# Performance work log

Hardware: AMD Instinct MI355X
Metric: run time of the kernel (lower is better)

Reference implementation:

```python
import jax, jax.numpy as jnp
import numpy as np

D_MODEL = 768
N_HEADS_CFG = 12
D_STATE = 32
D_CONV = 4
EXPAND = 2
HEADDIM = D_MODEL // N_HEADS_CFG          # 64
D_INNER = EXPAND * D_MODEL                # 1536
NHEADS = D_INNER // HEADDIM               # 24 (Mamba2 internal heads)
CONV_DIM = D_INNER + 2 * D_STATE          # 1600
D_IN_PROJ = 2 * D_INNER + 2 * D_STATE + NHEADS  # 3160
EPS = 1e-5
B_SZ, SEQ = 2, 512


def rmsnorm(x, w):
    return x * jax.lax.rsqrt(jnp.mean(x * x, axis=-1, keepdims=True) + EPS) * w


def mamba2(u, Wi, cw, cb, dtb, Alog, Dp, nw, Wo):
    """Mamba2 mixer: in_proj -> causal depthwise conv(silu) -> selective scan -> gated RMSNorm -> out_proj."""
    b, l, _ = u.shape
    zxbcdt = u @ Wi.T                                   # [b,l,d_in_proj]
    z, xBC, dt = jnp.split(zxbcdt, [D_INNER, D_INNER + CONV_DIM], axis=-1)
    # causal depthwise conv over time
    xBC = jnp.transpose(xBC, (0, 2, 1))                 # [b,c,l]
    xBC = jax.lax.conv_general_dilated(
        xBC, cw[:, None, :], window_strides=(1,),
        padding=[(D_CONV - 1, 0)], feature_group_count=CONV_DIM)
    xBC = jax.nn.silu(jnp.transpose(xBC + cb[None, :, None], (0, 2, 1)))
    x, Bm, Cm = jnp.split(xBC, [D_INNER, D_INNER + D_STATE], axis=-1)
    x = x.reshape(b, l, NHEADS, HEADDIM)                # [b,l,h,p]
    dt = jax.nn.softplus(dt + dtb)                      # [b,l,h]
    A = -jnp.exp(Alog)                                  # [h]
    a = jnp.exp(dt * A)                                 # decay [b,l,h]
    # dt * x outer B  -> [b,l,h,p,n]
    dBx = (dt[..., None, None] * x[..., None]) * Bm[:, :, None, None, :]

    def combine(e1, e2):
        a1, h1 = e1
        a2, h2 = e2
        return (a1 * a2, a2[..., None, None] * h1 + h2)

    _, h = jax.lax.associative_scan(combine, (a, dBx), axis=1)  # h: [b,l,h,p,n]
    y = jnp.einsum('blhpn,bln->blhp', h, Cm) + Dp[None, None, :, None] * x
    y = y.reshape(b, l, D_INNER)
    y = rmsnorm(y * jax.nn.silu(z), nw)                 # gated RMSNorm
    return y @ Wo.T                                     # [b,l,d_model]


def _mamba_params(key, scale=0.02):
    ks = jax.random.split(key, 6)
    return dict(
        in_w=jax.random.normal(ks[0], (D_IN_PROJ, D_MODEL), jnp.float32) * scale,
        conv_w=jax.random.normal(ks[1], (CONV_DIM, D_CONV), jnp.float32) * scale,
        conv_b=jnp.zeros((CONV_DIM,), jnp.float32),
        dt_bias=jax.random.uniform(ks[2], (NHEADS,), jnp.float32, -4.0, -1.0),
        A_log=jnp.log(jax.random.uniform(ks[3], (NHEADS,), jnp.float32, 1.0, 16.0)),
        D=jnp.ones((NHEADS,), jnp.float32),
        norm_w=jnp.ones((D_INNER,), jnp.float32),
        out_w=jax.random.normal(ks[4], (D_MODEL, D_INNER), jnp.float32) * scale,
    )


def setup_inputs() -> dict:
    key = jax.random.key(0)
    kx, kf, kb, ko = jax.random.split(key, 4)
    f = _mamba_params(kf)
    bw = _mamba_params(kb)
    return {
        'x': jax.random.normal(kx, (B_SZ, SEQ, D_MODEL), jnp.float32),
        'norm_w': jnp.ones((D_MODEL,), jnp.float32),
        'fwd_in_w': f['in_w'], 'fwd_conv_w': f['conv_w'], 'fwd_conv_b': f['conv_b'],
        'fwd_dt_bias': f['dt_bias'], 'fwd_A_log': f['A_log'], 'fwd_D': f['D'],
        'fwd_norm_w': f['norm_w'], 'fwd_out_w': f['out_w'],
        'bwd_in_w': bw['in_w'], 'bwd_conv_w': bw['conv_w'], 'bwd_conv_b': bw['conv_b'],
        'bwd_dt_bias': bw['dt_bias'], 'bwd_A_log': bw['A_log'], 'bwd_D': bw['D'],
        'bwd_norm_w': bw['norm_w'], 'bwd_out_w': bw['out_w'],
        'out_proj_w': jax.random.normal(ko, (D_MODEL, 2 * D_MODEL), jnp.float32) * 0.02,
    }


def reference(x, norm_w,
              fwd_in_w, fwd_conv_w, fwd_conv_b, fwd_dt_bias, fwd_A_log, fwd_D, fwd_norm_w, fwd_out_w,
              bwd_in_w, bwd_conv_w, bwd_conv_b, bwd_dt_bias, bwd_A_log, bwd_D, bwd_norm_w, bwd_out_w,
              out_proj_w):
    h = rmsnorm(x, norm_w)
    f_out = mamba2(h, fwd_in_w, fwd_conv_w, fwd_conv_b, fwd_dt_bias, fwd_A_log, fwd_D, fwd_norm_w, fwd_out_w)
    b_out = mamba2(h[:, ::-1], bwd_in_w, bwd_conv_w, bwd_conv_b, bwd_dt_bias, bwd_A_log, bwd_D, bwd_norm_w, bwd_out_w)[:, ::-1]
    return x + jnp.concatenate([f_out, b_out], axis=-1) @ out_proj_w.T
```

## Files before the change

### kernel.cpp

```cpp
#include <hip/hip_runtime.h>
#include <hip/hip_bf16.h>

#define DMODEL 768
#define DINNER 1536
#define DSTATE 32
#define NHEADS 24
#define HEADDIM 64
#define CONVDIM 1600
#define DINPROJ 3160
#define NPAD 3200
#define SEQ 512
#define MROWS 1024
#define CL 64
#define NCH 8

typedef __attribute__((ext_vector_type(8))) short bf16x8;
typedef __attribute__((ext_vector_type(4))) float f32x4;

__device__ __forceinline__ ushort f2bs(float v) {
  __hip_bfloat16 b = __float2bfloat16(v);
  return __builtin_bit_cast(unsigned short, b);
}

__device__ __forceinline__ void gld16(const void* g, const void* l) {
  __builtin_amdgcn_global_load_lds((const __attribute__((address_space(1))) void*)g,
                                   (__attribute__((address_space(3))) void*)l, 16, 0, 0);
}

__device__ __forceinline__ float block_reduce_sum(float v, float* ws4) {
#pragma unroll
  for (int o = 32; o > 0; o >>= 1) v += __shfl_xor(v, o, 64);
  int wid = threadIdx.x >> 6;
  if ((threadIdx.x & 63) == 0) ws4[wid] = v;
  __syncthreads();
  return ws4[0] + ws4[1] + ws4[2] + ws4[3];
}

__global__ __launch_bounds__(256) void f2b_all(
    const float* __restrict__ s0, const float* __restrict__ s1,
    const float* __restrict__ s2, const float* __restrict__ s3,
    const float* __restrict__ s4, ushort* __restrict__ d) {
  constexpr size_t NP_IN = (size_t)NPAD * DMODEL;
  constexpr size_t NE_IN = (size_t)DINPROJ * DMODEL;
  constexpr size_t NE_O = (size_t)DMODEL * DINNER;
  size_t i = ((size_t)blockIdx.x * 256 + threadIdx.x) * 4;
  const float* src;
  size_t off, ne;
  if (i < NP_IN) { src = s0; off = i; ne = NE_IN; }
  else if (i < 2 * NP_IN) { src = s1; off = i - NP_IN; ne = NE_IN; }
  else if (i < 2 * NP_IN + NE_O) { src = s2; off = i - 2 * NP_IN; ne = NE_O; }
  else if (i < 2 * NP_IN + 2 * NE_O) { src = s3; off = i - 2 * NP_IN - NE_O; ne = NE_O; }
  else if (i < 2 * NP_IN + 3 * NE_O) { src = s4; off = i - 2 * NP_IN - 2 * NE_O; ne = NE_O; }
  else return;
  ushort* dp = d + i;
  if (off + 3 < ne) {
    float4 v = *(const float4*)(src + off);
    dp[0] = f2bs(v.x); dp[1] = f2bs(v.y); dp[2] = f2bs(v.z); dp[3] = f2bs(v.w);
  } else {
#pragma unroll
    for (int j = 0; j < 4; ++j) dp[j] = (off + j < ne) ? f2bs(src[off + j]) : (ushort)0;
  }
}

__global__ __launch_bounds__(256) void rmsnorm_in_kernel(
    const float* __restrict__ x, const float* __restrict__ w, ushort* __restrict__ h) {
  __shared__ float ws4[4];
  int m = blockIdx.x;
  const float* xr = x + (size_t)m * DMODEL;
  float v[3];
  float ss = 0.f;
#pragma unroll
  for (int i = 0; i < 3; ++i) {
    v[i] = xr[threadIdx.x + i * 256];
    ss += v[i] * v[i];
  }
  ss = block_reduce_sum(ss, ws4);
  float sc = rsqrtf(ss / (float)DMODEL + 1e-5f);
  ushort* hr = h + (size_t)m * DMODEL;
#pragma unroll
  for (int i = 0; i < 3; ++i) {
    int c = threadIdx.x + i * 256;
    hr[c] = f2bs(v[i] * sc * w[c]);
  }
}

template <int BM, int BN, bool ADD_X, bool OUT_BF16>
__global__ __launch_bounds__(256) void gemm2(
    const ushort* __restrict__ A, int lda, size_t aZ,
    const ushort* __restrict__ Bw, int ldb, size_t bZ,
    void* __restrict__ Cout, int ldc, size_t cZ,
    const float* __restrict__ X, int ldx, int K) {
  constexpr int AG = BM / 16;
  constexpr int BG = BN / 16;
  constexpr int MR = BM / 32;
  constexpr int NR = BN / 32;
  __shared__ ushort As[2][BM * 32];
  __shared__ ushort Bs[2][BN * 32];
  const int t = threadIdx.x, w = t >> 6, l = t & 63;
  const int m0 = blockIdx.y * BM, n0 = blockIdx.x * BN;
  const int wr = w >> 1, wc = w & 1;
  const int fr = l & 15, fq = l >> 4;
  const int sr = l >> 2, sc2 = (l & 3) * 8;
  const ushort* Ap = A + (size_t)blockIdx.z * aZ;
  const ushort* Bp = Bw + (size_t)blockIdx.z * bZ;

  auto stage = [&](int bb, int k0) {
#pragma unroll
    for (int g = w; g < AG + BG; g += 4) {
      if (g < AG) {
        int row = g * 16 + sr;
        gld16(Ap + (size_t)(m0 + row) * lda + k0 + sc2, (const char*)&As[bb][0] + g * 1024);
      } else {
        int gg = g - AG;
        int row = gg * 16 + sr;
        gld16(Bp + (size_t)(n0 + row) * ldb + k0 + sc2, (const char*)&Bs[bb][0] + gg * 1024);
      }
    }
  };

  f32x4 acc[MR][NR];
#pragma unroll
  for (int m = 0; m < MR; ++m)
#pragma unroll
    for (int n = 0; n < NR; ++n) acc[m][n] = (f32x4){0.f, 0.f, 0.f, 0.f};

  stage(0, 0);
  __syncthreads();
  int cur = 0;
  const int nk = K / 32;
  for (int k = 0; k < nk; ++k) {
    if (k + 1 < nk) stage(cur ^ 1, (k + 1) * 32);
    bf16x8 af[MR], bfr[NR];
#pragma unroll
    for (int m = 0; m < MR; ++m)
      af[m] = *(const bf16x8*)&As[cur][(wr * (BM / 2) + m * 16 + fr) * 32 + fq * 8];
#pragma unroll
    for (int n = 0; n < NR; ++n)
      bfr[n] = *(const bf16x8*)&Bs[cur][(wc * (BN / 2) + n * 16 + fr) * 32 + fq * 8];
#pragma unroll
    for (int m = 0; m < MR; ++m)
#pragma unroll
      for (int n = 0; n < NR; ++n)
        acc[m][n] = __builtin_amdgcn_mfma_f32_16x16x32_bf16(af[m], bfr[n], acc[m][n], 0, 0, 0);
    __syncthreads();
    cur ^= 1;
  }

#pragma unroll
  for (int m = 0; m < MR; ++m) {
#pragma unroll
    for (int n = 0; n < NR; ++n) {
      int col = n0 + wc * (BN / 2) + n * 16 + fr;
#pragma unroll
      for (int j = 0; j < 4; ++j) {
        int row = m0 + wr * (BM / 2) + m * 16 + fq * 4 + j;
        float v = acc[m][n][j];
        if (ADD_X) v += X[(size_t)row * ldx + col];
        if (OUT_BF16)
          ((ushort*)Cout + (size_t)blockIdx.z * cZ)[(size_t)row * ldc + col] = f2bs(v);
        else
          ((float*)Cout + (size_t)blockIdx.z * cZ)[(size_t)row * ldc + col] = v;
      }
    }
  }
}

__global__ __launch_bounds__(256) void conv_dt_kernel(
    const float* __restrict__ zx,
    const float* __restrict__ cw0, const float* __restrict__ cb0,
    const float* __restrict__ dtb0, const float* __restrict__ Al0,
    const float* __restrict__ cw1, const float* __restrict__ cb1,
    const float* __restrict__ dtb1, const float* __restrict__ Al1,
    float* __restrict__ xbc, float* __restrict__ dta) {
  int m = blockIdx.x;
  int dir = blockIdx.y;
  int l = m & (SEQ - 1);
  const float* cw = dir ? cw1 : cw0;
  const float* cb = dir ? cb1 : cb0;
  const float* zrow = zx + (size_t)m * 6400 + dir * 3200 + DINNER;
  float* xo = xbc + ((size_t)dir * MROWS + m) * CONVDIM;
  for (int c = threadIdx.x; c < CONVDIM; c += 256) {
    float acc = cb[c];
    if (dir == 0) {
#pragma unroll
      for (int d = 0; d < 4; ++d) {
        if (l - d >= 0) acc = fmaf(zrow[-(size_t)d * 6400 + c], cw[c * 4 + 3 - d], acc);
      }
    } else {
#pragma unroll
      for (int d = 0; d < 4; ++d) {
        if (l + d < SEQ) acc = fmaf(zrow[(size_t)d * 6400 + c], cw[c * 4 + 3 - d], acc);
      }
    }
    xo[c] = acc / (1.f + expf(-acc));
  }
  if (threadIdx.x < NHEADS) {
    int hh = threadIdx.x;
    const float* dtb = dir ? dtb1 : dtb0;
    const float* Al = dir ? Al1 : Al0;
    float v = zx[(size_t)m * 6400 + dir * 3200 + DINNER + CONVDIM + hh] + dtb[hh];
    float dt = (v > 20.f) ? v : log1pf(expf(v));
    float A = -expf(Al[hh]);
    dta[((size_t)dir * MROWS + m) * 48 + hh] = dt;
    dta[((size_t)dir * MROWS + m) * 48 + NHEADS + hh] = expf(dt * A);
  }
}

__global__ __launch_bounds__(256) void scan_phase1(
    const float* __restrict__ xbc, const float* __restrict__ dta,
    float* __restrict__ sbuf, float* __restrict__ abuf) {
  __shared__ float xs[CL][64];
  __shared__ float bcs[CL][64];
  __shared__ float das[CL][2];
  int c = blockIdx.x, bh = blockIdx.y, dir = blockIdx.z;
  int b = bh / NHEADS, h = bh % NHEADS;
  int t = threadIdx.x, p = t >> 2, q = t & 3;
  const float* xb = xbc + ((size_t)dir * MROWS + b * SEQ) * CONVDIM;
  int lrow = t >> 4, lcol = (t & 15) * 4;
#pragma unroll
  for (int r = 0; r < 4; ++r) {
    int s = r * 16 + lrow;
    int tau = c * CL + s;
    int prow = dir ? (SEQ - 1 - tau) : tau;
    const float* rowp = xb + (size_t)prow * CONVDIM;
    *(float4*)&xs[s][lcol] = *(const float4*)(rowp + h * HEADDIM + lcol);
    *(float4*)&bcs[s][lcol] = *(const float4*)(rowp + DINNER + lcol);
  }
  if (t < 128) {
    int s = t >> 1, wsel = t & 1;
    int tau = c * CL + s;
    int prow = dir ? (SEQ - 1 - tau) : tau;
    das[s][wsel] = dta[((size_t)dir * MROWS + b * SEQ + prow) * 48 + wsel * NHEADS + h];
  }
  __syncthreads();
  float hst[8];
#pragma unroll
  for (int j = 0; j < 8; ++j) hst[j] = 0.f;
  float alpha = 1.f;
#pragma unroll 8
  for (int s = 0; s < CL; ++s) {
    float xp = xs[s][p];
    float dt_s = das[s][0], a_s = das[s][1];
    float cx = dt_s * xp;
    alpha *= a_s;
    float4 B0 = *(const float4*)&bcs[s][q * 8];
    float4 B1 = *(const float4*)&bcs[s][q * 8 + 4];
    float Bv[8] = {B0.x, B0.y, B0.z, B0.w, B1.x, B1.y, B1.z, B1.w};
#pragma unroll
    for (int j = 0; j < 8; ++j) hst[j] = fmaf(a_s, hst[j], cx * Bv[j]);
  }
  float* sp = sbuf + (((size_t)(dir * 48 + bh)) * NCH + c) * 2048 + p * 32 + q * 8;
#pragma unroll
  for (int j = 0; j < 8; ++j) sp[j] = hst[j];
  if (t == 0) abuf[(dir * 48 + bh) * NCH + c] = alpha;
}

__global__ __launch_bounds__(256) void scan_phase2(float* __restrict__ sbuf,
                                                   const float* __restrict__ abuf) {
  int g = blockIdx.x;
  int t = threadIdx.x;
  float run[8];
#pragma unroll
  for (int j = 0; j < 8; ++j) run[j] = 0.f;
  size_t base = (size_t)g * NCH * 2048 + t * 8;
  for (int c = 0; c < NCH; ++c) {
    float* sp = sbuf + base + (size_t)c * 2048;
    float4 s0 = *(const float4*)sp;
    float4 s1 = *(const float4*)(sp + 4);
    float al = abuf[g * NCH + c];
    float4 r0 = {run[0], run[1], run[2], run[3]};
    float4 r1 = {run[4], run[5], run[6], run[7]};
    *(float4*)sp = r0;
    *(float4*)(sp + 4) = r1;
    float sv[8] = {s0.x, s0.y, s0.z, s0.w, s1.x, s1.y, s1.z, s1.w};
#pragma unroll
    for (int j = 0; j < 8; ++j) run[j] = fmaf(al, run[j], sv[j]);
  }
}

__global__ __launch_bounds__(256) void scan_phase3(
    const float* __restrict__ xbc, const float* __restrict__ dta,
    const float* __restrict__ sbuf,
    const float* __restrict__ Dp0, const float* __restrict__ Dp1,
    float* __restrict__ y) {
  __shared__ float xs[CL][64];
  __shared__ float bcs[CL][64];
  __shared__ float das[CL][2];
  int c = blockIdx.x, bh = blockIdx.y, dir = blockIdx.z;
  int b = bh / NHEADS, h = bh % NHEADS;
  int t = threadIdx.x, p = t >> 2, q = t & 3;
  const float* xb = xbc + ((size_t)dir * MROWS + b * SEQ) * CONVDIM;
  int lrow = t >> 4, lcol = (t & 15) * 4;
#pragma unroll
  for (int r = 0; r < 4; ++r) {
    int s = r * 16 + lrow;
    int tau = c * CL + s;
    int prow = dir ? (SEQ - 1 - tau) : tau;
    const float* rowp = xb + (size_t)prow * CONVDIM;
    *(float4*)&xs[s][lcol] = *(const float4*)(rowp + h * HEADDIM + lcol);
    *(float4*)&bcs[s][lcol] = *(const float4*)(rowp + DINNER + lcol);
  }
  if (t < 128) {
    int s = t >> 1, wsel = t & 1;
    int tau = c * CL + s;
    int prow = dir ? (SEQ - 1 - tau) : tau;
    das[s][wsel] = dta[((size_t)dir * MROWS + b * SEQ + prow) * 48 + wsel * NHEADS + h];
  }
  float hst[8];
  {
    const float* sp = sbuf + (((size_t)(dir * 48 + bh)) * NCH + c) * 2048 + p * 32 + q * 8;
    float4 h0 = *(const float4*)sp;
    float4 h1 = *(const float4*)(sp + 4);
    hst[0] = h0.x; hst[1] = h0.y; hst[2] = h0.z; hst[3] = h0.w;
    hst[4] = h1.x; hst[5] = h1.y; hst[6] = h1.z; hst[7] = h1.w;
  }
  float Dv = (dir ? Dp1 : Dp0)[h];
  __syncthreads();
#pragma unroll 8
  for (int s = 0; s < CL; ++s) {
    float xp = xs[s][p];
    float dt_s = das[s][0], a_s = das[s][1];
    float cx = dt_s * xp;
    float4 B0 = *(const float4*)&bcs[s][q * 8];
    float4 B1 = *(const float4*)&bcs[s][q * 8 + 4];
    float4 C0 = *(const float4*)&bcs[s][32 + q * 8];
    float4 C1 = *(const float4*)&bcs[s][32 + q * 8 + 4];
    float Bv[8] = {B0.x, B0.y, B0.z, B0.w, B1.x, B1.y, B1.z, B1.w};
    float Cv[8] = {C0.x, C0.y, C0.z, C0.w, C1.x, C1.y, C1.z, C1.w};
    float acc = 0.f;
#pragma unroll
    for (int j = 0; j < 8; ++j) {
      hst[j] = fmaf(a_s, hst[j], cx * Bv[j]);
      acc = fmaf(hst[j], Cv[j], acc);
    }
    acc += __shfl_xor(acc, 1, 64);
    acc += __shfl_xor(acc, 2, 64);
    if (q == 0) {
      int tau = c * CL + s;
      int prow = dir ? (SEQ - 1 - tau) : tau;
      y[((size_t)dir * MROWS + b * SEQ + prow) * DINNER + h * HEADDIM + p] = fmaf(Dv, xp, acc);
    }
  }
}

__global__ __launch_bounds__(256) void gated_norm_kernel(
    const float* __restrict__ y,
    const float* __restrict__ zx,
    const float* __restrict__ nw0, const float* __restrict__ nw1,
    ushort* __restrict__ yn) {
  __shared__ float ws4[4];
  int m = blockIdx.x;
  int dir = blockIdx.y;
  const float* nw = dir ? nw1 : nw0;
  float g[6];
  float ss = 0.f;
#pragma unroll
  for (int i = 0; i < 6; ++i) {
    int c = threadIdx.x + i * 256;
    float yv = y[((size_t)dir * MROWS + m) * DINNER + c];
    float zv = zx[(size_t)m * 6400 + dir * 3200 + c];
    float gg = yv * (zv / (1.f + expf(-zv)));
    g[i] = gg;
    ss += gg * gg;
  }
  ss = block_reduce_sum(ss, ws4);
  float sc = rsqrtf(ss / (float)DINNER + 1e-5f);
#pragma unroll
  for (int i = 0; i < 6; ++i) {
    int c = threadIdx.x + i * 256;
    yn[((size_t)dir * MROWS + m) * DINNER + c] = f2bs(g[i] * sc * nw[c]);
  }
}

extern "C" void kernel_launch(void* const* d_in, const int* in_sizes, int n_in,
                              void* d_out, int out_size, void* d_ws, size_t ws_size,
                              hipStream_t stream) {
  const float* x = (const float*)d_in[0];
  const float* norm_w = (const float*)d_in[1];
  const float* in_w[2] = {(const float*)d_in[2], (const float*)d_in[10]};
  const float* conv_w[2] = {(const float*)d_in[3], (const float*)d_in[11]};
  const float* conv_b[2] = {(const float*)d_in[4], (const float*)d_in[12]};
  const float* dt_bias[2] = {(const float*)d_in[5], (const float*)d_in[13]};
  const float* A_log[2] = {(const float*)d_in[6], (const float*)d_in[14]};
  const float* Dp[2] = {(const float*)d_in[7], (const float*)d_in[15]};
  const float* nw[2] = {(const float*)d_in[8], (const float*)d_in[16]};
  const float* out_w[2] = {(const float*)d_in[9], (const float*)d_in[17]};
  const float* proj_w = (const float*)d_in[18];
  float* out = (float*)d_out;

  char* p = (char*)d_ws;
  float* zx = (float*)p;    p += (size_t)MROWS * 6400 * 4;
  float* xbc = (float*)p;   p += (size_t)2 * MROWS * CONVDIM * 4;
  float* dta = (float*)p;   p += (size_t)2 * MROWS * 48 * 4;
  float* y = (float*)p;     p += (size_t)2 * MROWS * DINNER * 4;
  float* sbuf = (float*)p;  p += (size_t)96 * NCH * 2048 * 4;
  float* abuf = (float*)p;  p += (size_t)96 * NCH * 4;
  ushort* h = (ushort*)p;   p += (size_t)MROWS * DMODEL * 2;
  ushort* yn = (ushort*)p;  p += (size_t)2 * MROWS * DINNER * 2;
  ushort* cat = (ushort*)p; p += (size_t)MROWS * DINNER * 2;
  ushort* wi = (ushort*)p;  p += (size_t)2 * NPAD * DMODEL * 2;
  ushort* wo = (ushort*)p;  p += (size_t)2 * DMODEL * DINNER * 2;
  ushort* wp = (ushort*)p;  p += (size_t)DMODEL * DINNER * 2;

  {
    size_t tot = 2 * (size_t)NPAD * DMODEL + 3 * (size_t)DMODEL * DINNER;
    f2b_all<<<(tot / 4 + 255) / 256, 256, 0, stream>>>(in_w[0], in_w[1], out_w[0], out_w[1],
                                                       proj_w, wi);
  }

  rmsnorm_in_kernel<<<MROWS, 256, 0, stream>>>(x, norm_w, h);

  {
    dim3 g(6400 / 128, MROWS / 128, 1);
    gemm2<128, 128, false, false><<<g, 256, 0, stream>>>(h, DMODEL, 0, wi, DMODEL, 0,
                                                         zx, 6400, 0, nullptr, 0, DMODEL);
  }

  conv_dt_kernel<<<dim3(MROWS, 2), 256, 0, stream>>>(
      zx, conv_w[0], conv_b[0], dt_bias[0], A_log[0],
      conv_w[1], conv_b[1], dt_bias[1], A_log[1], xbc, dta);

  scan_phase1<<<dim3(NCH, 48, 2), 256, 0, stream>>>(xbc, dta, sbuf, abuf);
  scan_phase2<<<96, 256, 0, stream>>>(sbuf, abuf);
  scan_phase3<<<dim3(NCH, 48, 2), 256, 0, stream>>>(xbc, dta, sbuf, Dp[0], Dp[1], y);

  gated_norm_kernel<<<dim3(MROWS, 2), 256, 0, stream>>>(y, zx, nw[0], nw[1], yn);

  {
    dim3 g(DMODEL / 64, MROWS / 128, 2);
    gemm2<128, 64, false, true><<<g, 256, 0, stream>>>(
        yn, DINNER, (size_t)MROWS * DINNER, wo, DINNER, (size_t)DMODEL * DINNER,
        cat, DINNER, (size_t)DMODEL, nullptr, 0, DINNER);
  }

  {
    dim3 g(DMODEL / 64, MROWS / 64, 1);
    gemm2<64, 64, true, false><<<g, 256, 0, stream>>>(cat, DINNER, 0, wp, DINNER, 0,
                                                      out, DMODEL, 0, x, DMODEL, DINNER);
  }
}
```

Baseline: 132.5 us.

## Merge prep kernels, fold scan phase2 into phase3, remap GEMM blocks, shrink tiles

The input RMSNorm now runs inside the weight-conversion kernel, and scan phase2 is removed: each phase3 block recomputes its incoming chunk state from the earlier chunks' partial states. The GEMM swizzles its block index so that consecutive blocks are spread across the grid (an XCD-style mapping). The in_proj and out_proj GEMMs move to smaller 64-row tiles for more blocks, and the phase1 state stores become vectorized. This removes two launches and the serial phase2 pass, at the cost of redundant prefix work in later chunks and smaller GEMM tiles with less reuse per block.

New measurement: 128.6 us. -2.9%, faster.

```diff
diff --git a/kernel.cpp b/kernel.cpp
--- a/kernel.cpp
+++ b/kernel.cpp
@@ -36,14 +36,36 @@
   return ws4[0] + ws4[1] + ws4[2] + ws4[3];
 }
 
-__global__ __launch_bounds__(256) void f2b_all(
+__global__ __launch_bounds__(256) void prep_kernel(
+    const float* __restrict__ x, const float* __restrict__ w, ushort* __restrict__ h,
     const float* __restrict__ s0, const float* __restrict__ s1,
     const float* __restrict__ s2, const float* __restrict__ s3,
     const float* __restrict__ s4, ushort* __restrict__ d) {
+  if (blockIdx.x < MROWS) {
+    __shared__ float ws4[4];
+    int m = blockIdx.x;
+    const float* xr = x + (size_t)m * DMODEL;
+    float v[3];
+    float ss = 0.f;
+#pragma unroll
+    for (int i = 0; i < 3; ++i) {
+      v[i] = xr[threadIdx.x + i * 256];
+      ss += v[i] * v[i];
+    }
+    ss = block_reduce_sum(ss, ws4);
+    float sc = rsqrtf(ss / (float)DMODEL + 1e-5f);
+    ushort* hr = h + (size_t)m * DMODEL;
+#pragma unroll
+    for (int i = 0; i < 3; ++i) {
+      int c = threadIdx.x + i * 256;
+      hr[c] = f2bs(v[i] * sc * w[c]);
+    }
+    return;
+  }
   constexpr size_t NP_IN = (size_t)NPAD * DMODEL;
   constexpr size_t NE_IN = (size_t)DINPROJ * DMODEL;
   constexpr size_t NE_O = (size_t)DMODEL * DINNER;
-  size_t i = ((size_t)blockIdx.x * 256 + threadIdx.x) * 4;
+  size_t i = (((size_t)blockIdx.x - MROWS) * 256 + threadIdx.x) * 4;
   const float* src;
   size_t off, ne;
   if (i < NP_IN) { src = s0; off = i; ne = NE_IN; }
@@ -62,30 +84,8 @@
   }
 }
 
-__global__ __launch_bounds__(256) void rmsnorm_in_kernel(
-    const float* __restrict__ x, const float* __restrict__ w, ushort* __restrict__ h) {
-  __shared__ float ws4[4];
-  int m = blockIdx.x;
-  const float* xr = x + (size_t)m * DMODEL;
-  float v[3];
-  float ss = 0.f;
-#pragma unroll
-  for (int i = 0; i < 3; ++i) {
-    v[i] = xr[threadIdx.x + i * 256];
-    ss += v[i] * v[i];
-  }
-  ss = block_reduce_sum(ss, ws4);
-  float sc = rsqrtf(ss / (float)DMODEL + 1e-5f);
-  ushort* hr = h + (size_t)m * DMODEL;
-#pragma unroll
-  for (int i = 0; i < 3; ++i) {
-    int c = threadIdx.x + i * 256;
-    hr[c] = f2bs(v[i] * sc * w[c]);
-  }
-}
-
 template <int BM, int BN, bool ADD_X, bool OUT_BF16>
-__global__ __launch_bounds__(256) void gemm2(
+__global__ __launch_bounds__(256) void gemm4(
     const ushort* __restrict__ A, int lda, size_t aZ,
     const ushort* __restrict__ Bw, int ldb, size_t bZ,
     void* __restrict__ Cout, int ldc, size_t cZ,
@@ -97,7 +97,15 @@
   __shared__ ushort As[2][BM * 32];
   __shared__ ushort Bs[2][BN * 32];
   const int t = threadIdx.x, w = t >> 6, l = t & 63;
-  const int m0 = blockIdx.y * BM, n0 = blockIdx.x * BN;
+  int bx, by;
+  {
+    int gx = gridDim.x, gy = gridDim.y;
+    int nwg = gx * gy;
+    int flat = blockIdx.y * gx + blockIdx.x;
+    int s = (flat & 7) * (nwg >> 3) + (flat >> 3);
+    bx = s / gy; by = s % gy;
+  }
+  const int m0 = by * BM, n0 = bx * BN;
   const int wr = w >> 1, wc = w & 1;
   const int fr = l & 15, fq = l >> 4;
   const int sr = l >> 2, sc2 = (l & 3) * 8;
@@ -107,14 +115,11 @@
   auto stage = [&](int bb, int k0) {
 #pragma unroll
     for (int g = w; g < AG + BG; g += 4) {
-      if (g < AG) {
-        int row = g * 16 + sr;
-        gld16(Ap + (size_t)(m0 + row) * lda + k0 + sc2, (const char*)&As[bb][0] + g * 1024);
-      } else {
-        int gg = g - AG;
-        int row = gg * 16 + sr;
-        gld16(Bp + (size_t)(n0 + row) * ldb + k0 + sc2, (const char*)&Bs[bb][0] + gg * 1024);
-      }
+      if (g < AG)
+        gld16(Ap + (size_t)(m0 + g * 16 + sr) * lda + k0 + sc2, (const char*)&As[bb][0] + g * 1024);
+      else
+        gld16(Bp + (size_t)(n0 + (g - AG) * 16 + sr) * ldb + k0 + sc2,
+              (const char*)&Bs[bb][0] + (g - AG) * 1024);
     }
   };
 
@@ -250,37 +255,14 @@
     for (int j = 0; j < 8; ++j) hst[j] = fmaf(a_s, hst[j], cx * Bv[j]);
   }
   float* sp = sbuf + (((size_t)(dir * 48 + bh)) * NCH + c) * 2048 + p * 32 + q * 8;
-#pragma unroll
-  for (int j = 0; j < 8; ++j) sp[j] = hst[j];
+  *(float4*)sp = (float4){hst[0], hst[1], hst[2], hst[3]};
+  *(float4*)(sp + 4) = (float4){hst[4], hst[5], hst[6], hst[7]};
   if (t == 0) abuf[(dir * 48 + bh) * NCH + c] = alpha;
 }
 
-__global__ __launch_bounds__(256) void scan_phase2(float* __restrict__ sbuf,
-                                                   const float* __restrict__ abuf) {
-  int g = blockIdx.x;
-  int t = threadIdx.x;
-  float run[8];
-#pragma unroll
-  for (int j = 0; j < 8; ++j) run[j] = 0.f;
-  size_t base = (size_t)g * NCH * 2048 + t * 8;
-  for (int c = 0; c < NCH; ++c) {
-    float* sp = sbuf + base + (size_t)c * 2048;
-    float4 s0 = *(const float4*)sp;
-    float4 s1 = *(const float4*)(sp + 4);
-    float al = abuf[g * NCH + c];
-    float4 r0 = {run[0], run[1], run[2], run[3]};
-    float4 r1 = {run[4], run[5], run[6], run[7]};
-    *(float4*)sp = r0;
-    *(float4*)(sp + 4) = r1;
-    float sv[8] = {s0.x, s0.y, s0.z, s0.w, s1.x, s1.y, s1.z, s1.w};
-#pragma unroll
-    for (int j = 0; j < 8; ++j) run[j] = fmaf(al, run[j], sv[j]);
-  }
-}
-
-__global__ __launch_bounds__(256) void scan_phase3(
+__global__ __launch_bounds__(256) void scan_phase3b(
     const float* __restrict__ xbc, const float* __restrict__ dta,
-    const float* __restrict__ sbuf,
+    const float* __restrict__ sbuf, const float* __restrict__ abuf,
     const float* __restrict__ Dp0, const float* __restrict__ Dp1,
     float* __restrict__ y) {
   __shared__ float xs[CL][64];
@@ -306,14 +288,20 @@
     int prow = dir ? (SEQ - 1 - tau) : tau;
     das[s][wsel] = dta[((size_t)dir * MROWS + b * SEQ + prow) * 48 + wsel * NHEADS + h];
   }
+
   float hst[8];
-  {
-    const float* sp = sbuf + (((size_t)(dir * 48 + bh)) * NCH + c) * 2048 + p * 32 + q * 8;
-    float4 h0 = *(const float4*)sp;
-    float4 h1 = *(const float4*)(sp + 4);
-    hst[0] = h0.x; hst[1] = h0.y; hst[2] = h0.z; hst[3] = h0.w;
-    hst[4] = h1.x; hst[5] = h1.y; hst[6] = h1.z; hst[7] = h1.w;
-  }
+#pragma unroll
+  for (int j = 0; j < 8; ++j) hst[j] = 0.f;
+  for (int cc = 0; cc < c; ++cc) {
+    const float* sp = sbuf + (((size_t)(dir * 48 + bh)) * NCH + cc) * 2048 + p * 32 + q * 8;
+    float4 s0 = *(const float4*)sp;
+    float4 s1 = *(const float4*)(sp + 4);
+    float al = abuf[(dir * 48 + bh) * NCH + cc];
+    float sv[8] = {s0.x, s0.y, s0.z, s0.w, s1.x, s1.y, s1.z, s1.w};
+#pragma unroll
+    for (int j = 0; j < 8; ++j) hst[j] = fmaf(al, hst[j], sv[j]);
+  }
+
   float Dv = (dir ? Dp1 : Dp0)[h];
   __syncthreads();
 #pragma unroll 8
@@ -404,16 +392,15 @@
 
   {
     size_t tot = 2 * (size_t)NPAD * DMODEL + 3 * (size_t)DMODEL * DINNER;
-    f2b_all<<<(tot / 4 + 255) / 256, 256, 0, stream>>>(in_w[0], in_w[1], out_w[0], out_w[1],
-                                                       proj_w, wi);
-  }
-
-  rmsnorm_in_kernel<<<MROWS, 256, 0, stream>>>(x, norm_w, h);
+    int fblocks = (int)((tot / 4 + 255) / 256);
+    prep_kernel<<<MROWS + fblocks, 256, 0, stream>>>(x, norm_w, h, in_w[0], in_w[1],
+                                                     out_w[0], out_w[1], proj_w, wi);
+  }
 
   {
-    dim3 g(6400 / 128, MROWS / 128, 1);
-    gemm2<128, 128, false, false><<<g, 256, 0, stream>>>(h, DMODEL, 0, wi, DMODEL, 0,
-                                                         zx, 6400, 0, nullptr, 0, DMODEL);
+    dim3 g(6400 / 128, MROWS / 64, 1);
+    gemm4<64, 128, false, false><<<g, 256, 0, stream>>>(h, DMODEL, 0, wi, DMODEL, 0,
+                                                        zx, 6400, 0, nullptr, 0, DMODEL);
   }
 
   conv_dt_kernel<<<dim3(MROWS, 2), 256, 0, stream>>>(
@@ -421,21 +408,20 @@
       conv_w[1], conv_b[1], dt_bias[1], A_log[1], xbc, dta);
 
   scan_phase1<<<dim3(NCH, 48, 2), 256, 0, stream>>>(xbc, dta, sbuf, abuf);
-  scan_phase2<<<96, 256, 0, stream>>>(sbuf, abuf);
-  scan_phase3<<<dim3(NCH, 48, 2), 256, 0, stream>>>(xbc, dta, sbuf, Dp[0], Dp[1], y);
+  scan_phase3b<<<dim3(NCH, 48, 2), 256, 0, stream>>>(xbc, dta, sbuf, abuf, Dp[0], Dp[1], y);
 
   gated_norm_kernel<<<dim3(MROWS, 2), 256, 0, stream>>>(y, zx, nw[0], nw[1], yn);
 
   {
-    dim3 g(DMODEL / 64, MROWS / 128, 2);
-    gemm2<128, 64, false, true><<<g, 256, 0, stream>>>(
+    dim3 g(DMODEL / 64, MROWS / 64, 2);
+    gemm4<64, 64, false, true><<<g, 256, 0, stream>>>(
         yn, DINNER, (size_t)MROWS * DINNER, wo, DINNER, (size_t)DMODEL * DINNER,
         cat, DINNER, (size_t)DMODEL, nullptr, 0, DINNER);
   }
 
   {
     dim3 g(DMODEL / 64, MROWS / 64, 1);
-    gemm2<64, 64, true, false><<<g, 256, 0, stream>>>(cat, DINNER, 0, wp, DINNER, 0,
+    gemm4<64, 64, true, false><<<g, 256, 0, stream>>>(cat, DINNER, 0, wp, DINNER, 0,
                                                       out, DMODEL, 0, x, DMODEL, DINNER);
   }
 }
```
